# Optimization experiments

Measured on AMD Instinct MI355X. Metric: run time of the kernel, lower is better.

The kernel has to match this reference:

```python
import jax, jax.numpy as jnp
import numpy as np

# Fixed 3x3 gaussian kernel from the original module (not learned)
_KERNEL = jnp.array([[0.03797616, 0.044863533, 0.03797616],
                     [0.044863533, 0.053,      0.044863533],
                     [0.03797616, 0.044863533, 0.03797616]], dtype=jnp.float32)


def _gaussian_con(x):
    # torch expands kernel to (C_out=C, C_in=C, 3, 3): every output channel is the
    # gaussian filter applied to the SUM over input channels (cross-channel mixing).
    C = x.shape[1]
    w = jnp.broadcast_to(_KERNEL, (C, C, 3, 3)).astype(x.dtype)
    return jax.lax.conv_general_dilated(
        x, w, window_strides=(1, 1), padding='SAME',
        dimension_numbers=('NCHW', 'OIHW', 'NCHW'))


def setup_inputs() -> dict:
    key = jax.random.key(0)
    k1, k2 = jax.random.split(key)
    B, C, H, W = 8, 3, 1024, 1024
    x = jax.random.uniform(k1, (B, C, H, W), dtype=jnp.float32)
    y = jax.random.uniform(k2, (B, C, H, W), dtype=jnp.float32)
    return {"x": x, "y": y}


def reference(x, y):
    B, C, W, H = x.shape  # original names x.size()[2]=width, [3]=heigh
    C1 = (0.01 * 255) ** 2
    C2 = (0.03 * 255) ** 2
    N = W * H  # pixels per channel
    denom = 3.0 * (N - 1)  # count starts at -1 in the original, then *3

    def step(carry, idx):
        xc, yc = carry
        # Original re-convolves the WHOLE batch each iteration (x = gaussion_con(x))
        xc = _gaussian_con(xc)
        yc = _gaussian_con(yc)
        xi = xc[idx]  # (3, W, H)
        yi = yc[idx]
        # mean over channels of per-channel means == global mean (equal-size channels)
        mean_x = xi.mean()
        mean_y = yi.mean()
        # unbiased (ddof=1) per-channel variance, averaged over the 3 channels
        std_x = jnp.var(xi, axis=(1, 2), ddof=1).mean()
        std_y = jnp.var(yi, axis=(1, 2), ddof=1).mean()
        # covariance-like term uses the GLOBAL means, summed over all channels/pixels
        conv = jnp.sum((xi - mean_x) * (yi - mean_y)) / denom
        one_turn = ((2 * mean_x * mean_y + C1) * (2 * conv + C2)) / (
            (mean_x ** 2 + mean_y ** 2 + C1) * (std_x ** 2 + std_y ** 2 + C2))
        return (xc, yc), one_turn

    (_, _), terms = jax.lax.scan(step, (x, y), jnp.arange(B))
    return terms.sum()
```

## Files before the change

kernel.cpp:

```cpp
#include <hip/hip_runtime.h>


typedef float v2f __attribute__((ext_vector_type(2)));
typedef float v4f __attribute__((ext_vector_type(4)));

#define BSTR 50

#define PC 0.19487473f
#define QC 0.23021731f

#define NSLOT 64

struct SharedMem {
  v2f buf[80 * BSTR];
  float Wt[9 * 17];
  double wred[4 * 5];
};

__global__ __launch_bounds__(256) void ssim_zero(double* acc) {
  for (int i = threadIdx.x; i < 8 * NSLOT * 5; i += 256) acc[i] = 0.0;
}

template <int H>
__device__ __forceinline__ void body(SharedMem& sm, int oy, int ox, int tr, int tc,
                                     const float* __restrict__ xp,
                                     const float* __restrict__ yp,
                                     double* __restrict__ accn) {
  constexpr int T = 2 * H + 1;
  constexpr int n = H - 1;
  constexpr int R0 = 8 - H, R1 = 71 + H;
  const int tid = threadIdx.x;

  if (tid <= H) {
    float* Wd = sm.Wt + tid * T;
    for (int k = 0; k < T; ++k) Wd[k] = (k == H) ? 1.f : 0.f;
    const int kmin = H - tid;
    for (int m = 0; m < H; ++m) {
      float prev = 0.f;
      for (int k = kmin; k < T; ++k) {
        const float cur = Wd[k];
        const float nxt = (k < T - 1) ? Wd[k + 1] : 0.f;
        Wd[k] = QC * cur + PC * (prev + nxt);
        prev = cur;
      }
    }
  }

  {
    constexpr int CC0 = (8 - H) >> 2, CC1 = (39 + H) >> 2;
    const size_t base = (size_t)n * 3145728u;
    for (int c = tid; c < 960; c += 256) {
      const int row = c / 12;
      const int c4 = c - row * 12;
      if (row < R0 || row > R1 || c4 < CC0 || c4 > CC1) continue;
      const int gy = oy + row - 8;
      const int gx0 = ox + c4 * 4 - 8;
      v4f sx = {0.f, 0.f, 0.f, 0.f}, sy = {0.f, 0.f, 0.f, 0.f};
      if (((unsigned)gy < 1024u) && ((unsigned)gx0 < 1024u)) {
        const size_t off = base + (size_t)gy * 1024u + (unsigned)gx0;
        const v4f* px = (const v4f*)(xp + off);
        const v4f* py = (const v4f*)(yp + off);
        sx = px[0] + px[262144] + px[524288];
        sy = py[0] + py[262144] + py[524288];
      }
      v4f* d = (v4f*)(sm.buf + row * BSTR + c4 * 4);
      d[0] = (v4f){sx.x, sy.x, sx.y, sy.y};
      d[1] = (v4f){sx.z, sy.z, sx.w, sy.w};
    }
  }
  __syncthreads();

  {
    const int g = tid >> 6;
    const int i0 = tid & 63;
    constexpr int I0 = (8 - H) >> 1, I1 = (15 + H) >> 1;
    const bool colEdge = (tc == 0) | (tc == 31);
    float cw[T];
    int A0[8], sg[8];
    if (colEdge) {
#pragma unroll
      for (int j = 0; j < 8; ++j) {
        const int gx = ox + g * 8 + j;
        int dd = H, rv = 0;
        if (gx < H) dd = gx;
        else if (gx > 1023 - H) { dd = 1023 - gx; rv = 1; }
        A0[j] = dd * T + (rv ? 2 * H : 0);
        sg[j] = rv ? -1 : 1;
      }
    } else {
#pragma unroll
      for (int k = 0; k < T; ++k) cw[k] = sm.Wt[H * T + k];
    }

    auto htask = [&](v2f* o, int r) {
      const v4f* s4 = (const v4f*)(sm.buf + r * BSTR + g * 8);
      v2f win[24];
#pragma unroll
      for (int i = I0; i <= I1; ++i) {
        const v4f t = s4[i];
        win[2 * i] = (v2f){t.x, t.y};
        win[2 * i + 1] = (v2f){t.z, t.w};
      }
      if (!colEdge) {
#pragma unroll
        for (int k = 0; k < T; ++k)
#pragma unroll
          for (int j = 0; j < 8; ++j)
            o[j] += cw[k] * win[j + k + 8 - H];
      } else {
#pragma unroll
        for (int j = 0; j < 8; ++j)
          for (int k = 0; k < T; ++k)
            o[j] += sm.Wt[A0[j] + sg[j] * k] * win[j + k + 8 - H];
      }
    };

    v2f o1[8] = {}, o2[8] = {};
    const int r2 = i0 + 64;
    const bool val1 = (i0 >= R0);
    const bool val2 = (r2 <= R1);
    if (val1) htask(o1, i0);
    if (val2) htask(o2, r2);
    __syncthreads();
    if (val1) {
      v4f* d = (v4f*)(sm.buf + i0 * BSTR + g * 8 + 8);
#pragma unroll
      for (int jj = 0; jj < 4; ++jj)
        d[jj] = (v4f){o1[2 * jj].x, o1[2 * jj].y, o1[2 * jj + 1].x, o1[2 * jj + 1].y};
    }
    if (val2) {
      v4f* d = (v4f*)(sm.buf + r2 * BSTR + g * 8 + 8);
#pragma unroll
      for (int jj = 0; jj < 4; ++jj)
        d[jj] = (v4f){o2[2 * jj].x, o2[2 * jj].y, o2[2 * jj + 1].x, o2[2 * jj + 1].y};
    }
  }
  __syncthreads();

  constexpr float scales[8] = {1.f, 3.f, 9.f, 27.f, 81.f, 243.f, 729.f, 2187.f};
  const float scale = scales[n];
  float sA = 0.f, sB = 0.f, sAA = 0.f, sBB = 0.f, sAB = 0.f;
  {
    const int jt = tid & 31;
    const int iv = tid >> 5;
    constexpr int C0 = 8 - H, C1 = 15 + H;
    v2f vwin[24];
#pragma unroll
    for (int c = C0; c <= C1; ++c)
      vwin[c] = sm.buf[(8 * iv + c) * BSTR + 8 + jt];
    v2f o[8] = {};
    const bool rowEdge = (tr == 0) | (tr == 15);
    if (!rowEdge) {
      float cw2[T];
#pragma unroll
      for (int k = 0; k < T; ++k) cw2[k] = sm.Wt[H * T + k];
#pragma unroll
      for (int k = 0; k < T; ++k)
#pragma unroll
        for (int rr = 0; rr < 8; ++rr)
          o[rr] += cw2[k] * vwin[rr + k + 8 - H];
    } else {
#pragma unroll
      for (int rr = 0; rr < 8; ++rr) {
        const int gy = oy + 8 * iv + rr;
        int dd = H, rv = 0;
        if (gy < H) dd = gy;
        else if (gy > 1023 - H) { dd = 1023 - gy; rv = 1; }
        const int A0 = dd * T + (rv ? 2 * H : 0);
        const int s = rv ? -1 : 1;
        for (int k = 0; k < T; ++k)
          o[rr] += sm.Wt[A0 + s * k] * vwin[rr + k + 8 - H];
      }
    }
#pragma unroll
    for (int rr = 0; rr < 8; ++rr) {
      const float A = scale * o[rr].x;
      const float B = scale * o[rr].y;
      sA += A; sB += B;
      sAA += A * A; sBB += B * B; sAB += A * B;
    }
  }

  double v[5] = {(double)sA, (double)sB, (double)sAA, (double)sBB, (double)sAB};
#pragma unroll
  for (int off = 32; off > 0; off >>= 1) {
#pragma unroll
    for (int k = 0; k < 5; ++k) v[k] += __shfl_down(v[k], off, 64);
  }
  const int lane = tid & 63, wv = tid >> 6;
  if (lane == 0) {
#pragma unroll
    for (int k = 0; k < 5; ++k) sm.wred[wv * 5 + k] = v[k];
  }
  __syncthreads();
  if (tid == 0) {
#pragma unroll
    for (int k = 0; k < 5; ++k)
      atomicAdd(&accn[k], sm.wred[k] + sm.wred[5 + k] + sm.wred[10 + k] + sm.wred[15 + k]);
  }
}

__global__ __launch_bounds__(256, 5) void ssim_main(const float* __restrict__ xp,
                                                    const float* __restrict__ yp,
                                                    double* __restrict__ acc) {
  __shared__ SharedMem sm;
  const int bid = blockIdx.x;
  const int n = bid & 7;
  const int tile = bid >> 3;
  const int tc = tile & 31;
  const int tr = tile >> 5;
  const int oy = tr * 64;
  const int ox = tc * 32;
  const int slot = tile & (NSLOT - 1);
  double* accn = acc + (n * NSLOT + slot) * 5;
  switch (n) {
    case 0: body<1>(sm, oy, ox, tr, tc, xp, yp, accn); break;
    case 1: body<2>(sm, oy, ox, tr, tc, xp, yp, accn); break;
    case 2: body<3>(sm, oy, ox, tr, tc, xp, yp, accn); break;
    case 3: body<4>(sm, oy, ox, tr, tc, xp, yp, accn); break;
    case 4: body<5>(sm, oy, ox, tr, tc, xp, yp, accn); break;
    case 5: body<6>(sm, oy, ox, tr, tc, xp, yp, accn); break;
    case 6: body<7>(sm, oy, ox, tr, tc, xp, yp, accn); break;
    default: body<8>(sm, oy, ox, tr, tc, xp, yp, accn); break;
  }
}

__global__ __launch_bounds__(256) void ssim_final(const double* __restrict__ acc,
                                                  float* __restrict__ out) {
  __shared__ double terms[8];
  const int tid = threadIdx.x;
  const int s = tid >> 5;
  const int l = tid & 31;
  double v[5];
#pragma unroll
  for (int k = 0; k < 5; ++k)
    v[k] = acc[(s * NSLOT + l) * 5 + k] + acc[(s * NSLOT + l + 32) * 5 + k];
#pragma unroll
  for (int off = 16; off > 0; off >>= 1) {
#pragma unroll
    for (int k = 0; k < 5; ++k) v[k] += __shfl_down(v[k], off, 32);
  }
  if (l == 0) {
    const double C1 = 6.5025;
    const double C2 = 58.5225;
    const double N = 1048576.0;
    const double mA = v[0] / N, mB = v[1] / N;
    const double varA = (v[2] - N * mA * mA) / (N - 1.0);
    const double varB = (v[3] - N * mB * mB) / (N - 1.0);
    const double cov  = (v[4] - N * mA * mB) / (N - 1.0);
    terms[s] = ((2.0 * mA * mB + C1) * (2.0 * cov + C2)) /
               ((mA * mA + mB * mB + C1) * (varA * varA + varB * varB + C2));
  }
  __syncthreads();
  if (tid == 0) {
    double tot = 0.0;
    for (int i = 0; i < 8; ++i) tot += terms[i];
    out[0] = (float)tot;
  }
}

extern "C" void kernel_launch(void* const* d_in, const int* in_sizes, int n_in,
                              void* d_out, int out_size, void* d_ws, size_t ws_size,
                              hipStream_t stream) {
  const float* x = (const float*)d_in[0];
  const float* y = (const float*)d_in[1];
  double* acc = (double*)d_ws;
  float* out = (float*)d_out;

  ssim_zero<<<1, 256, 0, stream>>>(acc);
  ssim_main<<<4096, 256, 0, stream>>>(x, y, acc);
  ssim_final<<<1, 256, 0, stream>>>(acc, out);
}
```

Before: 245.9 us.

## Halve tile height, precompute filter tables in constant memory, raise occupancy

Shrinks each block's output tile from 64x32 to 32x32 and doubles the grid. Each thread now does one horizontal row and four vertical outputs, which cuts registers and shared memory so the launch bound can rise to 8 blocks per CU. The per-block iterative weight construction is replaced by compile-time tables in constant memory, and those tables are copied to shared memory only for edge tiles. The cost is a larger halo fraction per tile, meaning more redundant global loads and horizontal work.

```diff
diff --git a/kernel.cpp b/kernel.cpp
--- a/kernel.cpp
+++ b/kernel.cpp
@@ -11,10 +11,35 @@
 
 #define NSLOT 64
 
+struct WtTables { float w[8][153]; };
+static constexpr WtTables make_tables() {
+  WtTables t{};
+  for (int H = 1; H <= 8; ++H) {
+    const int T = 2 * H + 1;
+    for (int d = 0; d <= H; ++d) {
+      float Wd[17] = {};
+      for (int k = 0; k < T; ++k) Wd[k] = (k == H) ? 1.f : 0.f;
+      const int kmin = H - d;
+      for (int m = 0; m < H; ++m) {
+        float prev = 0.f;
+        for (int k = kmin; k < T; ++k) {
+          const float cur = Wd[k];
+          const float nxt = (k < T - 1) ? Wd[k + 1] : 0.f;
+          Wd[k] = QC * cur + PC * (prev + nxt);
+          prev = cur;
+        }
+      }
+      for (int k = 0; k < T; ++k) t.w[H - 1][d * T + k] = Wd[k];
+    }
+  }
+  return t;
+}
+__constant__ WtTables WTAB = make_tables();
+
 struct SharedMem {
-  v2f buf[80 * BSTR];
-  float Wt[9 * 17];
+  v2f buf[48 * BSTR];
   double wred[4 * 5];
+  float Wt[153];
 };
 
 __global__ __launch_bounds__(256) void ssim_zero(double* acc) {
@@ -28,28 +53,15 @@
                                      double* __restrict__ accn) {
   constexpr int T = 2 * H + 1;
   constexpr int n = H - 1;
-  constexpr int R0 = 8 - H, R1 = 71 + H;
+  constexpr int R0 = 8 - H, R1 = 39 + H;
   const int tid = threadIdx.x;
-
-  if (tid <= H) {
-    float* Wd = sm.Wt + tid * T;
-    for (int k = 0; k < T; ++k) Wd[k] = (k == H) ? 1.f : 0.f;
-    const int kmin = H - tid;
-    for (int m = 0; m < H; ++m) {
-      float prev = 0.f;
-      for (int k = kmin; k < T; ++k) {
-        const float cur = Wd[k];
-        const float nxt = (k < T - 1) ? Wd[k + 1] : 0.f;
-        Wd[k] = QC * cur + PC * (prev + nxt);
-        prev = cur;
-      }
-    }
-  }
+  const bool rowEdge = (tr == 0) | (tr == 31);
+  const bool colEdge = (tc == 0) | (tc == 31);
 
   {
     constexpr int CC0 = (8 - H) >> 2, CC1 = (39 + H) >> 2;
     const size_t base = (size_t)n * 3145728u;
-    for (int c = tid; c < 960; c += 256) {
+    for (int c = tid; c < 576; c += 256) {
       const int row = c / 12;
       const int c4 = c - row * 12;
       if (row < R0 || row > R1 || c4 < CC0 || c4 > CC1) continue;
@@ -68,32 +80,19 @@
       d[1] = (v4f){sx.z, sy.z, sx.w, sy.w};
     }
   }
+  if (rowEdge | colEdge) {
+    for (int i = tid; i < (H + 1) * T; i += 256) sm.Wt[i] = WTAB.w[n][i];
+  }
   __syncthreads();
 
   {
     const int g = tid >> 6;
     const int i0 = tid & 63;
     constexpr int I0 = (8 - H) >> 1, I1 = (15 + H) >> 1;
-    const bool colEdge = (tc == 0) | (tc == 31);
-    float cw[T];
-    int A0[8], sg[8];
-    if (colEdge) {
-#pragma unroll
-      for (int j = 0; j < 8; ++j) {
-        const int gx = ox + g * 8 + j;
-        int dd = H, rv = 0;
-        if (gx < H) dd = gx;
-        else if (gx > 1023 - H) { dd = 1023 - gx; rv = 1; }
-        A0[j] = dd * T + (rv ? 2 * H : 0);
-        sg[j] = rv ? -1 : 1;
-      }
-    } else {
-#pragma unroll
-      for (int k = 0; k < T; ++k) cw[k] = sm.Wt[H * T + k];
-    }
-
-    auto htask = [&](v2f* o, int r) {
-      const v4f* s4 = (const v4f*)(sm.buf + r * BSTR + g * 8);
+    const bool val = (i0 >= R0) & (i0 <= R1);
+    v2f o[8] = {};
+    if (val) {
+      const v4f* s4 = (const v4f*)(sm.buf + i0 * BSTR + g * 8);
       v2f win[24];
 #pragma unroll
       for (int i = I0; i <= I1; ++i) {
@@ -103,36 +102,35 @@
       }
       if (!colEdge) {
 #pragma unroll
-        for (int k = 0; k < T; ++k)
+        for (int k = 0; k < T; ++k) {
+          const float cw = WTAB.w[n][H * T + k];
 #pragma unroll
           for (int j = 0; j < 8; ++j)
-            o[j] += cw[k] * win[j + k + 8 - H];
+            o[j] += cw * win[j + k + 8 - H];
+        }
       } else {
+        int A0[8], sg[8];
+#pragma unroll
+        for (int j = 0; j < 8; ++j) {
+          const int gx = ox + g * 8 + j;
+          int dd = H, rv = 0;
+          if (gx < H) dd = gx;
+          else if (gx > 1023 - H) { dd = 1023 - gx; rv = 1; }
+          A0[j] = dd * T + (rv ? 2 * H : 0);
+          sg[j] = rv ? -1 : 1;
+        }
 #pragma unroll
         for (int j = 0; j < 8; ++j)
           for (int k = 0; k < T; ++k)
             o[j] += sm.Wt[A0[j] + sg[j] * k] * win[j + k + 8 - H];
       }
-    };
-
-    v2f o1[8] = {}, o2[8] = {};
-    const int r2 = i0 + 64;
-    const bool val1 = (i0 >= R0);
-    const bool val2 = (r2 <= R1);
-    if (val1) htask(o1, i0);
-    if (val2) htask(o2, r2);
+    }
     __syncthreads();
-    if (val1) {
+    if (val) {
       v4f* d = (v4f*)(sm.buf + i0 * BSTR + g * 8 + 8);
 #pragma unroll
       for (int jj = 0; jj < 4; ++jj)
-        d[jj] = (v4f){o1[2 * jj].x, o1[2 * jj].y, o1[2 * jj + 1].x, o1[2 * jj + 1].y};
-    }
-    if (val2) {
-      v4f* d = (v4f*)(sm.buf + r2 * BSTR + g * 8 + 8);
-#pragma unroll
-      for (int jj = 0; jj < 4; ++jj)
-        d[jj] = (v4f){o2[2 * jj].x, o2[2 * jj].y, o2[2 * jj + 1].x, o2[2 * jj + 1].y};
+        d[jj] = (v4f){o[2 * jj].x, o[2 * jj].y, o[2 * jj + 1].x, o[2 * jj + 1].y};
     }
   }
   __syncthreads();
@@ -143,26 +141,24 @@
   {
     const int jt = tid & 31;
     const int iv = tid >> 5;
-    constexpr int C0 = 8 - H, C1 = 15 + H;
-    v2f vwin[24];
+    constexpr int C0 = 8 - H, C1 = 11 + H;
+    v2f vwin[20];
 #pragma unroll
     for (int c = C0; c <= C1; ++c)
-      vwin[c] = sm.buf[(8 * iv + c) * BSTR + 8 + jt];
-    v2f o[8] = {};
-    const bool rowEdge = (tr == 0) | (tr == 15);
+      vwin[c] = sm.buf[(4 * iv + c) * BSTR + 8 + jt];
+    v2f o[4] = {};
     if (!rowEdge) {
-      float cw2[T];
-#pragma unroll
-      for (int k = 0; k < T; ++k) cw2[k] = sm.Wt[H * T + k];
-#pragma unroll
-      for (int k = 0; k < T; ++k)
-#pragma unroll
-        for (int rr = 0; rr < 8; ++rr)
-          o[rr] += cw2[k] * vwin[rr + k + 8 - H];
+#pragma unroll
+      for (int k = 0; k < T; ++k) {
+        const float cw = WTAB.w[n][H * T + k];
+#pragma unroll
+        for (int rr = 0; rr < 4; ++rr)
+          o[rr] += cw * vwin[rr + k + 8 - H];
+      }
     } else {
 #pragma unroll
-      for (int rr = 0; rr < 8; ++rr) {
-        const int gy = oy + 8 * iv + rr;
+      for (int rr = 0; rr < 4; ++rr) {
+        const int gy = oy + 4 * iv + rr;
         int dd = H, rv = 0;
         if (gy < H) dd = gy;
         else if (gy > 1023 - H) { dd = 1023 - gy; rv = 1; }
@@ -173,7 +169,7 @@
       }
     }
 #pragma unroll
-    for (int rr = 0; rr < 8; ++rr) {
+    for (int rr = 0; rr < 4; ++rr) {
       const float A = scale * o[rr].x;
       const float B = scale * o[rr].y;
       sA += A; sB += B;
@@ -200,7 +196,7 @@
   }
 }
 
-__global__ __launch_bounds__(256, 5) void ssim_main(const float* __restrict__ xp,
+__global__ __launch_bounds__(256, 8) void ssim_main(const float* __restrict__ xp,
                                                     const float* __restrict__ yp,
                                                     double* __restrict__ acc) {
   __shared__ SharedMem sm;
@@ -209,7 +205,7 @@
   const int tile = bid >> 3;
   const int tc = tile & 31;
   const int tr = tile >> 5;
-  const int oy = tr * 64;
+  const int oy = tr * 32;
   const int ox = tc * 32;
   const int slot = tile & (NSLOT - 1);
   double* accn = acc + (n * NSLOT + slot) * 5;
@@ -268,6 +264,6 @@
   float* out = (float*)d_out;
 
   ssim_zero<<<1, 256, 0, stream>>>(acc);
-  ssim_main<<<4096, 256, 0, stream>>>(x, y, acc);
+  ssim_main<<<8192, 256, 0, stream>>>(x, y, acc);
   ssim_final<<<1, 256, 0, stream>>>(acc, out);
 }
```

Result: slower. 275.5 us (+12.0%).
